# Optimization experiments

Hardware: AMD Instinct MI355X
Metric: run time of the kernel (lower is better)

Reference implementation:

```python
import jax, jax.numpy as jnp
import numpy as np

B, T, E, H = 64, 512, 256, 128


def setup_inputs() -> dict:
    key = jax.random.key(0)
    ks = jax.random.split(key, 7)
    s = 1.0 / np.sqrt(H)  # PyTorch LSTM default init range
    inputs = jax.random.normal(ks[0], (B, T, E), jnp.float32)
    labels = jax.random.randint(ks[1], (B, T), 0, H)
    W_ih = jax.random.uniform(ks[2], (4 * H, E), jnp.float32, -s, s)
    W_hh = jax.random.uniform(ks[3], (4 * H, H), jnp.float32, -s, s)
    b_ih = jax.random.uniform(ks[4], (4 * H,), jnp.float32, -s, s)
    b_hh = jax.random.uniform(ks[5], (4 * H,), jnp.float32, -s, s)
    transition = jax.random.uniform(ks[6], (H, H), jnp.float32)  # torch.rand
    return {"inputs": inputs, "labels": labels, "W_ih": W_ih, "W_hh": W_hh,
            "b_ih": b_ih, "b_hh": b_hh, "transition": transition}


def _lstm(x, W_ih, W_hh, b_ih, b_hh):
    # x: (T, B, E) -> hs: (T, B, H). PyTorch gate order: i, f, g, o.
    Bn = x.shape[1]
    Hn = W_hh.shape[1]

    def step(carry, xt):
        h, c = carry
        g = xt @ W_ih.T + b_ih + h @ W_hh.T + b_hh  # (B, 4H)
        i, f, gg, o = jnp.split(g, 4, axis=-1)
        c = jax.nn.sigmoid(f) * c + jax.nn.sigmoid(i) * jnp.tanh(gg)
        h = jax.nn.sigmoid(o) * jnp.tanh(c)
        return (h, c), h

    h0 = jnp.zeros((Bn, Hn), x.dtype)
    (_, _), hs = jax.lax.scan(step, (h0, h0), x)
    return hs


def reference(inputs, labels, W_ih, W_hh, b_ih, b_hh, transition):
    x = inputs.transpose(1, 0, 2)  # (T, B, E)
    trans = jax.nn.softmax(transition, axis=1)  # row-softmax transition
    hs = _lstm(x, W_ih, W_hh, b_ih, b_hh)  # (T, B, H)
    Hbth = jax.nn.softmax(hs, axis=2).transpose(1, 0, 2)  # (B, T, H)

    # gold-path score Pr: emissions at gold tags + transition scores
    emit = jnp.take_along_axis(Hbth, labels[:, :, None], axis=2)[..., 0].sum(axis=1)  # (B,)
    tr_score = trans[labels[:, :-1], labels[:, 1:]].sum(axis=1)  # (B,)
    Pr = emit + tr_score

    # CRF forward algorithm (partition score Ps) via scan over time
    pre0 = Hbth[:, 0, :] + trans[0]  # (B, H)

    def crf_step(pre, h_t):
        # Z[b, i, j] = pre[b, i] + trans[i, j] + h_t[b, j]
        Z = pre[:, :, None] + trans[None] + h_t[:, None, :]
        return jax.nn.logsumexp(Z, axis=1), None

    pre, _ = jax.lax.scan(crf_step, pre0, Hbth[:, 1:, :].transpose(1, 0, 2))
    Ps = jax.nn.logsumexp(pre + trans[-1][None, :], axis=1)  # (B,)

    return (Ps - Pr).sum()
```

## Files before the change

### kernel.cpp

```cpp
#include <hip/hip_runtime.h>
#include <hip/hip_bf16.h>
#include <cstdint>

#define BB 64
#define TT 512
#define EE 256
#define HH 128
#define G4 512

typedef _Float16 half2_t __attribute__((ext_vector_type(2)));
typedef _Float16 f16x4 __attribute__((ext_vector_type(4)));
typedef _Float16 f16x8 __attribute__((ext_vector_type(8)));
typedef float f32x4 __attribute__((ext_vector_type(4)));

#define BC(x) __builtin_bit_cast(half2_t, x)

#define BAR() asm volatile("s_waitcnt lgkmcnt(0)\n\ts_barrier" ::: "memory")

__device__ __forceinline__ float fdot2f(half2_t a, half2_t b, float c) {
#if defined(__has_builtin)
#if __has_builtin(__builtin_amdgcn_fdot2)
  return __builtin_amdgcn_fdot2(a, b, c, false);
#else
  return c + (float)a[0] * (float)b[0] + (float)a[1] * (float)b[1];
#endif
#else
  return c + (float)a[0] * (float)b[0] + (float)a[1] * (float)b[1];
#endif
}

__device__ __forceinline__ float rcp_(float x) { return __builtin_amdgcn_rcpf(x); }
__device__ __forceinline__ float sigmoid_(float x) { return rcp_(1.f + __expf(-x)); }
__device__ __forceinline__ float tanh_(float x) {
  float ax = fabsf(x);
  float e = __expf(-2.f * ax);
  float r = (1.f - e) * rcp_(1.f + e);
  return copysignf(r, x);
}

__device__ __forceinline__ float readlane_f(float x, int lane) {
#if defined(__has_builtin)
#if __has_builtin(__builtin_amdgcn_readlane)
  return __builtin_bit_cast(float, __builtin_amdgcn_readlane(__builtin_bit_cast(int, x), lane));
#else
  return __shfl(x, lane);
#endif
#else
  return __shfl(x, lane);
#endif
}

#if defined(__has_builtin)
#if __has_builtin(__builtin_amdgcn_update_dpp)
#define HAVE_DPP 1
#endif
#endif

__device__ __forceinline__ float wave_sum64_bcast(float x) {
#ifdef HAVE_DPP
#define DPP_ADD(ctrl)                                                          \
  {                                                                            \
    int _t = __builtin_amdgcn_update_dpp(0, __builtin_bit_cast(int, x), ctrl,  \
                                         0xf, 0xf, true);                      \
    x += __builtin_bit_cast(float, _t);                                        \
  }
  DPP_ADD(0x111)
  DPP_ADD(0x112)
  DPP_ADD(0x114)
  DPP_ADD(0x118)
  DPP_ADD(0x142)
  DPP_ADD(0x143)
#undef DPP_ADD
  return readlane_f(x, 63);
#else
#pragma unroll
  for (int s = 1; s <= 32; s <<= 1) x += __shfl_xor(x, s);
  return x;
#endif
}

__device__ __host__ __forceinline__ int permj(int j) {
  return ((j & 127) << 2) | (j >> 7);
}

__global__ __launch_bounds__(128) void prep_kernel(
    const float* __restrict__ transition, const float* __restrict__ W_ih,
    float* __restrict__ trans, _Float16* __restrict__ W16) {
  const int bid = blockIdx.x, t = threadIdx.x;
  if (bid < 128) {
    __shared__ float red[2];
    float v = transition[bid * HH + t];
    float m = v;
#pragma unroll
    for (int s = 32; s >= 1; s >>= 1) m = fmaxf(m, __shfl_xor(m, s));
    if ((t & 63) == 0) red[t >> 6] = m;
    __syncthreads();
    m = fmaxf(red[0], red[1]);
    float e = __expf(v - m);
    float s = e;
#pragma unroll
    for (int k = 32; k >= 1; k >>= 1) s += __shfl_xor(s, k);
    __syncthreads();
    if ((t & 63) == 0) red[t >> 6] = s;
    __syncthreads();
    trans[bid * HH + t] = e * rcp_(red[0] + red[1]);
  } else {
    const int base = (bid - 128) * 1024 + t * 8;
    const int row = base >> 8;
    const int col = base & 255;
    float4 v0 = *(const float4*)(W_ih + base);
    float4 v1 = *(const float4*)(W_ih + base + 4);
    f16x8 h;
    h[0] = (_Float16)v0.x; h[1] = (_Float16)v0.y;
    h[2] = (_Float16)v0.z; h[3] = (_Float16)v0.w;
    h[4] = (_Float16)v1.x; h[5] = (_Float16)v1.y;
    h[6] = (_Float16)v1.z; h[7] = (_Float16)v1.w;
    *(f16x8*)(W16 + (size_t)permj(row) * EE + col) = h;
  }
}

__global__ __launch_bounds__(256) void gemm_in(
    const float* __restrict__ A, const _Float16* __restrict__ W16,
    const float* __restrict__ b_ih, const float* __restrict__ b_hh,
    float* __restrict__ out) {
  __shared__ _Float16 As[64][264];
  const int t = threadIdx.x;
  const int m0 = blockIdx.x * 64;
  const int n0 = blockIdx.y * 256;
  {
    const int c4 = t & 63, r0 = t >> 6;
#pragma unroll
    for (int p = 0; p < 16; ++p) {
      const int row = r0 + 4 * p;
      float4 v = *(const float4*)(A + (size_t)(m0 + row) * EE + c4 * 4);
      f16x4 h;
      h[0] = (_Float16)v.x; h[1] = (_Float16)v.y;
      h[2] = (_Float16)v.z; h[3] = (_Float16)v.w;
      *(f16x4*)&As[row][c4 * 4] = h;
    }
  }
  __syncthreads();
  const int w = t >> 6, L = t & 63;
  const int lrow = L & 15, quad = L >> 4, lk = quad * 8;
  f32x4 acc[4][4] = {};
  const _Float16* Wbase = W16 + (size_t)(n0 + w * 64) * EE;
#pragma unroll
  for (int kc = 0; kc < 8; ++kc) {
    f16x8 a[4], bf[4];
#pragma unroll
    for (int mf = 0; mf < 4; ++mf)
      a[mf] = *(const f16x8*)&As[mf * 16 + lrow][kc * 32 + lk];
#pragma unroll
    for (int nf = 0; nf < 4; ++nf)
      bf[nf] = *(const f16x8*)(Wbase + (size_t)(nf * 16 + lrow) * EE + kc * 32 + lk);
#pragma unroll
    for (int mf = 0; mf < 4; ++mf)
#pragma unroll
      for (int nf = 0; nf < 4; ++nf)
        acc[mf][nf] = __builtin_amdgcn_mfma_f32_16x16x32_f16(a[mf], bf[nf], acc[mf][nf], 0, 0, 0);
  }
#pragma unroll
  for (int nf = 0; nf < 4; ++nf) {
    const int j = n0 + w * 64 + nf * 16 + lrow;
    const int jo = ((j & 3) << 7) | (j >> 2);
    const float bias = b_ih[jo] + b_hh[jo];
#pragma unroll
    for (int mf = 0; mf < 4; ++mf) {
#pragma unroll
      for (int r = 0; r < 4; ++r) {
        const int m = m0 + mf * 16 + quad * 4 + r;
        out[(size_t)m * G4 + j] = acc[mf][nf][r] + bias;
      }
    }
  }
}

__global__ __launch_bounds__(512, 1) void lstm_crf(
    const float* __restrict__ precomp, const float* __restrict__ Whh,
    const float* __restrict__ trans, const int* __restrict__ labels,
    float* __restrict__ out_b) {
  const int b = blockIdx.x, t = threadIdx.x;
  const int w = t >> 6, l = t & 63, q = l >> 4, l15 = l & 15;
  const int tf_a = l15 & 3;
  const int gg = l15 >> 2;
  const int ua = 16 * w + 4 * tf_a + q;
  const int g2 = t >> 7, jj = t & 127;

  __shared__ __align__(16) _Float16 h_lds[2][HH];
  __shared__ __align__(16) _Float16 E_lds[HH];
  __shared__ __align__(16) float act[G4];
  __shared__ __align__(16) float Spart[G4];
  __shared__ int lab[TT];

  f16x8 wfr[4][4];
#pragma unroll
  for (int tf = 0; tf < 4; ++tf) {
    const int rowp = 16 * (4 * w + tf) + l15;
    const int u = rowp >> 2, g = rowp & 3;
    const float* src = Whh + (size_t)(g * HH + u) * HH;
#pragma unroll
    for (int kt = 0; kt < 4; ++kt) {
      const float* s8 = src + kt * 32 + q * 8;
      float4 v0 = *(const float4*)s8;
      float4 v1 = *(const float4*)(s8 + 4);
      f16x8 h8;
      h8[0] = (_Float16)v0.x; h8[1] = (_Float16)v0.y;
      h8[2] = (_Float16)v0.z; h8[3] = (_Float16)v0.w;
      h8[4] = (_Float16)v1.x; h8[5] = (_Float16)v1.y;
      h8[6] = (_Float16)v1.z; h8[7] = (_Float16)v1.w;
      wfr[tf][kt] = h8;
    }
  }
  half2_t et[16];
#pragma unroll
  for (int a = 0; a < 16; ++a) {
    float e0 = __expf(trans[(g2 * 32 + 2 * a) * HH + jj]);
    float e1 = __expf(trans[(g2 * 32 + 2 * a + 1) * HH + jj]);
    half2_t h2; h2[0] = (_Float16)e0; h2[1] = (_Float16)e1;
    et[a] = h2;
  }
  lab[t] = labels[b * TT + t];
  if (t < HH) { h_lds[0][t] = (_Float16)0.f; E_lds[t] = (_Float16)0.f; }

  float tr0x = 0.f, tr0y = 0.f, tr127x = 0.f, tr127y = 0.f;
  if (t < 64) {
    float2 v0 = *(const float2*)(trans + 2 * t);
    float2 v1 = *(const float2*)(trans + 127 * HH + 2 * t);
    tr0x = v0.x; tr0y = v0.y; tr127x = v1.x; tr127y = v1.y;
  }
  float c0 = 0.f, c1 = 0.f, preA = 0.f, preB = 0.f, mused = 0.f, emit = 0.f;

  const float* pcb = precomp + (size_t)b * TT * G4 + 64 * w + 4 * q;
  f32x4 pc_cur[4], pc_nxt[4];
#pragma unroll
  for (int tf = 0; tf < 4; ++tf) pc_cur[tf] = *(const f32x4*)(pcb + 16 * tf);
  __syncthreads();

#pragma unroll 1
  for (int step = 0; step < TT; ++step) {
    const int pr = step & 1;
    const int sn = (step < TT - 1) ? step + 1 : step;
#pragma unroll
    for (int tf = 0; tf < 4; ++tf)
      pc_nxt[tf] = *(const f32x4*)(pcb + (size_t)sn * G4 + 16 * tf);
    const f16x8 hb0 = *(const f16x8*)&h_lds[pr][q * 8];
    const f16x8 hb1 = *(const f16x8*)&h_lds[pr][32 + q * 8];
    const f16x8 hb2 = *(const f16x8*)&h_lds[pr][64 + q * 8];
    const f16x8 hb3 = *(const f16x8*)&h_lds[pr][96 + q * 8];
    f32x4 a0 = pc_cur[0], a1 = pc_cur[1], a2 = pc_cur[2], a3 = pc_cur[3];
    a0 = __builtin_amdgcn_mfma_f32_16x16x32_f16(wfr[0][0], hb0, a0, 0, 0, 0);
    a1 = __builtin_amdgcn_mfma_f32_16x16x32_f16(wfr[1][0], hb0, a1, 0, 0, 0);
    a2 = __builtin_amdgcn_mfma_f32_16x16x32_f16(wfr[2][0], hb0, a2, 0, 0, 0);
    a3 = __builtin_amdgcn_mfma_f32_16x16x32_f16(wfr[3][0], hb0, a3, 0, 0, 0);
    a0 = __builtin_amdgcn_mfma_f32_16x16x32_f16(wfr[0][1], hb1, a0, 0, 0, 0);
    a1 = __builtin_amdgcn_mfma_f32_16x16x32_f16(wfr[1][1], hb1, a1, 0, 0, 0);
    a2 = __builtin_amdgcn_mfma_f32_16x16x32_f16(wfr[2][1], hb1, a2, 0, 0, 0);
    a3 = __builtin_amdgcn_mfma_f32_16x16x32_f16(wfr[3][1], hb1, a3, 0, 0, 0);
    a0 = __builtin_amdgcn_mfma_f32_16x16x32_f16(wfr[0][2], hb2, a0, 0, 0, 0);
    a1 = __builtin_amdgcn_mfma_f32_16x16x32_f16(wfr[1][2], hb2, a1, 0, 0, 0);
    a2 = __builtin_amdgcn_mfma_f32_16x16x32_f16(wfr[2][2], hb2, a2, 0, 0, 0);
    a3 = __builtin_amdgcn_mfma_f32_16x16x32_f16(wfr[3][2], hb2, a3, 0, 0, 0);
    a0 = __builtin_amdgcn_mfma_f32_16x16x32_f16(wfr[0][3], hb3, a0, 0, 0, 0);
    a1 = __builtin_amdgcn_mfma_f32_16x16x32_f16(wfr[1][3], hb3, a1, 0, 0, 0);
    a2 = __builtin_amdgcn_mfma_f32_16x16x32_f16(wfr[2][3], hb3, a2, 0, 0, 0);
    a3 = __builtin_amdgcn_mfma_f32_16x16x32_f16(wfr[3][3], hb3, a3, 0, 0, 0);
    float s0 = 0.f, s1 = 0.f;
    const float4* ev4 = (const float4*)E_lds + g2 * 4;
#pragma unroll
    for (int ec = 0; ec < 4; ++ec) {
      float4 eb = ev4[ec];
      s0 = fdot2f(et[4 * ec + 0], BC(eb.x), s0);
      s1 = fdot2f(et[4 * ec + 1], BC(eb.y), s1);
      s0 = fdot2f(et[4 * ec + 2], BC(eb.z), s0);
      s1 = fdot2f(et[4 * ec + 3], BC(eb.w), s1);
    }
    const f32x4 asel = (tf_a == 0) ? a0 : (tf_a == 1) ? a1 : (tf_a == 2) ? a2 : a3;
    const float gv = (gg == 0) ? asel[0] : (gg == 1) ? asel[1]
                   : (gg == 2) ? asel[2] : asel[3];
    const bool isg = (gg == 2);
    const float yy = isg ? (-2.f * fabsf(gv)) : (-gv);
    const float exv = __expf(yy);
    const float num = isg ? (1.f - exv) : 1.f;
    float av = num * rcp_(1.f + exv);
    av = isg ? copysignf(av, gv) : av;
    act[gg * HH + ua] = av;
    Spart[t] = s0 + s1;
    BAR();
    if (t < 64) {
      const float2* a2p = (const float2*)act;
      float2 I = a2p[t], F = a2p[64 + t], G = a2p[128 + t], O = a2p[192 + t];
      c0 = F.x * c0 + I.x * G.x;
      c1 = F.y * c1 + I.y * G.y;
      const float h0 = O.x * tanh_(c0), h1 = O.y * tanh_(c1);
      const float e0 = __expf(h0), e1 = __expf(h1);
      const float denom = wave_sum64_bcast(e0 + e1);
      const float rinv = rcp_(denom);
      const float p0 = e0 * rinv, p1 = e1 * rinv;
      const float2* s2p = (const float2*)Spart;
      float2 Sq0 = s2p[t], Sq1 = s2p[64 + t], Sq2 = s2p[128 + t], Sq3 = s2p[192 + t];
      const float Sa = (Sq0.x + Sq1.x) + (Sq2.x + Sq3.x);
      const float Sb = (Sq0.y + Sq1.y) + (Sq2.y + Sq3.y);
      const float lgSa = __logf(Sa), lgSb = __logf(Sb);
      const float lgS0 = readlane_f(lgSa, 0);
      const int lb = lab[step];
      const float Mnext = (step == 0) ? 0.f : (mused + lgS0);
      preA = p0 + ((step == 0) ? tr0x : (mused + lgSa));
      preB = p1 + ((step == 0) ? tr0y : (mused + lgSb));
      if (2 * t == lb) emit += p0;
      if (2 * t + 1 == lb) emit += p1;
      half2_t Eh;
      Eh[0] = (_Float16)__expf(preA - Mnext);
      Eh[1] = (_Float16)__expf(preB - Mnext);
      *(half2_t*)&E_lds[2 * t] = Eh;
      half2_t Hh;
      Hh[0] = (_Float16)h0; Hh[1] = (_Float16)h1;
      *(half2_t*)&h_lds[pr ^ 1][2 * t] = Hh;
      mused = Mnext;
    }
    BAR();
#pragma unroll
    for (int tf = 0; tf < 4; ++tf) pc_cur[tf] = pc_nxt[tf];
  }
  if (t < 64) {
    float v0 = preA + tr127x, v1 = preB + tr127y;
    float m = fmaxf(v0, v1);
#pragma unroll
    for (int s = 1; s <= 32; s <<= 1) m = fmaxf(m, __shfl_xor(m, s));
    float ex = __expf(v0 - m) + __expf(v1 - m);
    float em = emit;
#pragma unroll
    for (int s = 1; s <= 32; s <<= 1) {
      ex += __shfl_xor(ex, s);
      em += __shfl_xor(em, s);
    }
    if (t == 0) out_b[b] = m + __logf(ex) - em;
  }
}

__global__ __launch_bounds__(512) void finalize_kernel(
    const float* __restrict__ trans, const int* __restrict__ labels,
    const float* __restrict__ out_b, float* __restrict__ d_out) {
  const int t = threadIdx.x;
  float a = 0.f;
  if (t < TT - 1) {
    for (int b = 0; b < BB; ++b) {
      const int l0 = labels[b * TT + t];
      const int l1 = labels[b * TT + t + 1];
      a += trans[l0 * HH + l1];
    }
  }
  float x = ((t < BB) ? out_b[t] : 0.f) - a;
  __shared__ float red[8];
#pragma unroll
  for (int s = 32; s >= 1; s >>= 1) x += __shfl_xor(x, s);
  if ((t & 63) == 0) red[t >> 6] = x;
  __syncthreads();
  if (t == 0) {
    float s = 0.f;
#pragma unroll
    for (int i = 0; i < 8; ++i) s += red[i];
    d_out[0] = s;
  }
}

extern "C" void kernel_launch(void* const* d_in, const int* in_sizes, int n_in,
                              void* d_out, int out_size, void* d_ws, size_t ws_size,
                              hipStream_t stream) {
  const float* inputs = (const float*)d_in[0];
  const int* labels = (const int*)d_in[1];
  const float* W_ih = (const float*)d_in[2];
  const float* W_hh = (const float*)d_in[3];
  const float* b_ih = (const float*)d_in[4];
  const float* b_hh = (const float*)d_in[5];
  const float* transition = (const float*)d_in[6];

  char* ws = (char*)d_ws;
  float* precomp = (float*)ws;
  float* trans = (float*)(ws + 67108864);
  _Float16* W16 = (_Float16*)(ws + 67108864 + 65536);
  float* out_b = (float*)(ws + 67108864 + 65536 + 262144);

  prep_kernel<<<256, 128, 0, stream>>>(transition, W_ih, trans, W16);
  gemm_in<<<dim3(512, 2), 256, 0, stream>>>(inputs, W16, b_ih, b_hh, precomp);
  lstm_crf<<<64, 512, 0, stream>>>(precomp, W_hh, trans, labels, out_b);
  finalize_kernel<<<1, 512, 0, stream>>>(trans, labels, out_b, (float*)d_out);
}
```

Measured before the change: 563.1 us.

## Split LSTM and CRF into dedicated waves, pipelined with one barrier per step

The fused kernel gets two extra waves that run the CRF forward recursion one timestep behind the LSTM waves, so the two recurrences overlap. Each step now needs a single barrier instead of two. The LSTM cell update is done in-register with DPP lane shifts across the gate lanes, which removes the act/Spart LDS round trip and the single-wave serial cell update. The costs are 64 half2 transition registers per CRF lane, an extra pipeline step, and a 4-deep h ring buffer in both fp16 and fp32.

```diff
diff --git a/kernel.cpp b/kernel.cpp
--- a/kernel.cpp
+++ b/kernel.cpp
@@ -30,7 +30,6 @@
 }
 
 __device__ __forceinline__ float rcp_(float x) { return __builtin_amdgcn_rcpf(x); }
-__device__ __forceinline__ float sigmoid_(float x) { return rcp_(1.f + __expf(-x)); }
 __device__ __forceinline__ float tanh_(float x) {
   float ax = fabsf(x);
   float e = __expf(-2.f * ax);
@@ -54,6 +53,14 @@
 #if __has_builtin(__builtin_amdgcn_update_dpp)
 #define HAVE_DPP 1
 #endif
+#endif
+
+#ifdef HAVE_DPP
+#define DPP_SHL(dst, src, N)                                                   \
+  dst = __builtin_bit_cast(float, __builtin_amdgcn_update_dpp(                 \
+            0, __builtin_bit_cast(int, src), 0x100 | (N), 0xf, 0xf, true))
+#else
+#define DPP_SHL(dst, src, N) dst = __shfl((src), (threadIdx.x & 63) + (N))
 #endif
 
 __device__ __forceinline__ float wave_sum64_bcast(float x) {
@@ -175,7 +182,7 @@
   }
 }
 
-__global__ __launch_bounds__(512, 1) void lstm_crf(
+__global__ __launch_bounds__(640, 1) void lstm_crf(
     const float* __restrict__ precomp, const float* __restrict__ Whh,
     const float* __restrict__ trans, const int* __restrict__ labels,
     float* __restrict__ out_b) {
@@ -183,158 +190,175 @@
   const int w = t >> 6, l = t & 63, q = l >> 4, l15 = l & 15;
   const int tf_a = l15 & 3;
   const int gg = l15 >> 2;
-  const int ua = 16 * w + 4 * tf_a + q;
-  const int g2 = t >> 7, jj = t & 127;
-
-  __shared__ __align__(16) _Float16 h_lds[2][HH];
-  __shared__ __align__(16) _Float16 E_lds[HH];
-  __shared__ __align__(16) float act[G4];
-  __shared__ __align__(16) float Spart[G4];
+  const bool isL = (w < 8);
+  const int cw = w - 8;
+  const int j = cw * 64 + l;
+
+  __shared__ __align__(16) _Float16 h16[4][HH];
+  __shared__ __align__(16) float h32[4][HH];
+  __shared__ __align__(16) _Float16 E16[2][HH];
+  __shared__ float Mld[2][2];
+  __shared__ float fin[8];
   __shared__ int lab[TT];
 
   f16x8 wfr[4][4];
-#pragma unroll
-  for (int tf = 0; tf < 4; ++tf) {
-    const int rowp = 16 * (4 * w + tf) + l15;
-    const int u = rowp >> 2, g = rowp & 3;
-    const float* src = Whh + (size_t)(g * HH + u) * HH;
-#pragma unroll
-    for (int kt = 0; kt < 4; ++kt) {
-      const float* s8 = src + kt * 32 + q * 8;
-      float4 v0 = *(const float4*)s8;
-      float4 v1 = *(const float4*)(s8 + 4);
-      f16x8 h8;
-      h8[0] = (_Float16)v0.x; h8[1] = (_Float16)v0.y;
-      h8[2] = (_Float16)v0.z; h8[3] = (_Float16)v0.w;
-      h8[4] = (_Float16)v1.x; h8[5] = (_Float16)v1.y;
-      h8[6] = (_Float16)v1.z; h8[7] = (_Float16)v1.w;
-      wfr[tf][kt] = h8;
-    }
-  }
-  half2_t et[16];
-#pragma unroll
-  for (int a = 0; a < 16; ++a) {
-    float e0 = __expf(trans[(g2 * 32 + 2 * a) * HH + jj]);
-    float e1 = __expf(trans[(g2 * 32 + 2 * a + 1) * HH + jj]);
-    half2_t h2; h2[0] = (_Float16)e0; h2[1] = (_Float16)e1;
-    et[a] = h2;
-  }
-  lab[t] = labels[b * TT + t];
-  if (t < HH) { h_lds[0][t] = (_Float16)0.f; E_lds[t] = (_Float16)0.f; }
-
-  float tr0x = 0.f, tr0y = 0.f, tr127x = 0.f, tr127y = 0.f;
-  if (t < 64) {
-    float2 v0 = *(const float2*)(trans + 2 * t);
-    float2 v1 = *(const float2*)(trans + 127 * HH + 2 * t);
-    tr0x = v0.x; tr0y = v0.y; tr127x = v1.x; tr127y = v1.y;
-  }
-  float c0 = 0.f, c1 = 0.f, preA = 0.f, preB = 0.f, mused = 0.f, emit = 0.f;
-
-  const float* pcb = precomp + (size_t)b * TT * G4 + 64 * w + 4 * q;
   f32x4 pc_cur[4], pc_nxt[4];
-#pragma unroll
-  for (int tf = 0; tf < 4; ++tf) pc_cur[tf] = *(const f32x4*)(pcb + 16 * tf);
+  const float* pcb = nullptr;
+  float c = 0.f;
+  half2_t et[64];
+  float tr0 = 0.f, tr127 = 0.f, pre = 0.f, emit = 0.f;
+
+  if (isL) {
+#pragma unroll
+    for (int tf = 0; tf < 4; ++tf) {
+      const int rowp = 16 * (4 * w + tf) + l15;
+      const int u = rowp >> 2, g = rowp & 3;
+      const float* src = Whh + (size_t)(g * HH + u) * HH;
+#pragma unroll
+      for (int kt = 0; kt < 4; ++kt) {
+        const float* s8 = src + kt * 32 + q * 8;
+        float4 v0 = *(const float4*)s8;
+        float4 v1 = *(const float4*)(s8 + 4);
+        f16x8 h8;
+        h8[0] = (_Float16)v0.x; h8[1] = (_Float16)v0.y;
+        h8[2] = (_Float16)v0.z; h8[3] = (_Float16)v0.w;
+        h8[4] = (_Float16)v1.x; h8[5] = (_Float16)v1.y;
+        h8[6] = (_Float16)v1.z; h8[7] = (_Float16)v1.w;
+        wfr[tf][kt] = h8;
+      }
+    }
+    pcb = precomp + (size_t)b * TT * G4 + 64 * w + 4 * q;
+#pragma unroll
+    for (int tf = 0; tf < 4; ++tf) pc_cur[tf] = *(const f32x4*)(pcb + 16 * tf);
+  } else {
+#pragma unroll
+    for (int i = 0; i < 64; ++i) {
+      float e0 = __expf(trans[(2 * i) * HH + j]);
+      float e1 = __expf(trans[(2 * i + 1) * HH + j]);
+      half2_t h2; h2[0] = (_Float16)e0; h2[1] = (_Float16)e1;
+      et[i] = h2;
+    }
+    tr0 = trans[j];
+    tr127 = trans[127 * HH + j];
+  }
+  if (t < TT) lab[t] = labels[b * TT + t];
+  if (t < HH) { h16[0][t] = (_Float16)0.f; h32[0][t] = 0.f; }
   __syncthreads();
 
 #pragma unroll 1
-  for (int step = 0; step < TT; ++step) {
-    const int pr = step & 1;
-    const int sn = (step < TT - 1) ? step + 1 : step;
-#pragma unroll
-    for (int tf = 0; tf < 4; ++tf)
-      pc_nxt[tf] = *(const f32x4*)(pcb + (size_t)sn * G4 + 16 * tf);
-    const f16x8 hb0 = *(const f16x8*)&h_lds[pr][q * 8];
-    const f16x8 hb1 = *(const f16x8*)&h_lds[pr][32 + q * 8];
-    const f16x8 hb2 = *(const f16x8*)&h_lds[pr][64 + q * 8];
-    const f16x8 hb3 = *(const f16x8*)&h_lds[pr][96 + q * 8];
-    f32x4 a0 = pc_cur[0], a1 = pc_cur[1], a2 = pc_cur[2], a3 = pc_cur[3];
-    a0 = __builtin_amdgcn_mfma_f32_16x16x32_f16(wfr[0][0], hb0, a0, 0, 0, 0);
-    a1 = __builtin_amdgcn_mfma_f32_16x16x32_f16(wfr[1][0], hb0, a1, 0, 0, 0);
-    a2 = __builtin_amdgcn_mfma_f32_16x16x32_f16(wfr[2][0], hb0, a2, 0, 0, 0);
-    a3 = __builtin_amdgcn_mfma_f32_16x16x32_f16(wfr[3][0], hb0, a3, 0, 0, 0);
-    a0 = __builtin_amdgcn_mfma_f32_16x16x32_f16(wfr[0][1], hb1, a0, 0, 0, 0);
-    a1 = __builtin_amdgcn_mfma_f32_16x16x32_f16(wfr[1][1], hb1, a1, 0, 0, 0);
-    a2 = __builtin_amdgcn_mfma_f32_16x16x32_f16(wfr[2][1], hb1, a2, 0, 0, 0);
-    a3 = __builtin_amdgcn_mfma_f32_16x16x32_f16(wfr[3][1], hb1, a3, 0, 0, 0);
-    a0 = __builtin_amdgcn_mfma_f32_16x16x32_f16(wfr[0][2], hb2, a0, 0, 0, 0);
-    a1 = __builtin_amdgcn_mfma_f32_16x16x32_f16(wfr[1][2], hb2, a1, 0, 0, 0);
-    a2 = __builtin_amdgcn_mfma_f32_16x16x32_f16(wfr[2][2], hb2, a2, 0, 0, 0);
-    a3 = __builtin_amdgcn_mfma_f32_16x16x32_f16(wfr[3][2], hb2, a3, 0, 0, 0);
-    a0 = __builtin_amdgcn_mfma_f32_16x16x32_f16(wfr[0][3], hb3, a0, 0, 0, 0);
-    a1 = __builtin_amdgcn_mfma_f32_16x16x32_f16(wfr[1][3], hb3, a1, 0, 0, 0);
-    a2 = __builtin_amdgcn_mfma_f32_16x16x32_f16(wfr[2][3], hb3, a2, 0, 0, 0);
-    a3 = __builtin_amdgcn_mfma_f32_16x16x32_f16(wfr[3][3], hb3, a3, 0, 0, 0);
-    float s0 = 0.f, s1 = 0.f;
-    const float4* ev4 = (const float4*)E_lds + g2 * 4;
-#pragma unroll
-    for (int ec = 0; ec < 4; ++ec) {
-      float4 eb = ev4[ec];
-      s0 = fdot2f(et[4 * ec + 0], BC(eb.x), s0);
-      s1 = fdot2f(et[4 * ec + 1], BC(eb.y), s1);
-      s0 = fdot2f(et[4 * ec + 2], BC(eb.z), s0);
-      s1 = fdot2f(et[4 * ec + 3], BC(eb.w), s1);
-    }
-    const f32x4 asel = (tf_a == 0) ? a0 : (tf_a == 1) ? a1 : (tf_a == 2) ? a2 : a3;
-    const float gv = (gg == 0) ? asel[0] : (gg == 1) ? asel[1]
-                   : (gg == 2) ? asel[2] : asel[3];
-    const bool isg = (gg == 2);
-    const float yy = isg ? (-2.f * fabsf(gv)) : (-gv);
-    const float exv = __expf(yy);
-    const float num = isg ? (1.f - exv) : 1.f;
-    float av = num * rcp_(1.f + exv);
-    av = isg ? copysignf(av, gv) : av;
-    act[gg * HH + ua] = av;
-    Spart[t] = s0 + s1;
+  for (int s = 0; s <= TT; ++s) {
+    if (isL) {
+      if (s < TT) {
+        const int sn = (s < TT - 1) ? s + 1 : s;
+#pragma unroll
+        for (int tf = 0; tf < 4; ++tf)
+          pc_nxt[tf] = *(const f32x4*)(pcb + (size_t)sn * G4 + 16 * tf);
+        const int rs = s & 3;
+        const f16x8 hb0 = *(const f16x8*)&h16[rs][q * 8];
+        const f16x8 hb1 = *(const f16x8*)&h16[rs][32 + q * 8];
+        const f16x8 hb2 = *(const f16x8*)&h16[rs][64 + q * 8];
+        const f16x8 hb3 = *(const f16x8*)&h16[rs][96 + q * 8];
+        f32x4 a0 = pc_cur[0], a1 = pc_cur[1], a2 = pc_cur[2], a3 = pc_cur[3];
+        a0 = __builtin_amdgcn_mfma_f32_16x16x32_f16(wfr[0][0], hb0, a0, 0, 0, 0);
+        a1 = __builtin_amdgcn_mfma_f32_16x16x32_f16(wfr[1][0], hb0, a1, 0, 0, 0);
+        a2 = __builtin_amdgcn_mfma_f32_16x16x32_f16(wfr[2][0], hb0, a2, 0, 0, 0);
+        a3 = __builtin_amdgcn_mfma_f32_16x16x32_f16(wfr[3][0], hb0, a3, 0, 0, 0);
+        a0 = __builtin_amdgcn_mfma_f32_16x16x32_f16(wfr[0][1], hb1, a0, 0, 0, 0);
+        a1 = __builtin_amdgcn_mfma_f32_16x16x32_f16(wfr[1][1], hb1, a1, 0, 0, 0);
+        a2 = __builtin_amdgcn_mfma_f32_16x16x32_f16(wfr[2][1], hb1, a2, 0, 0, 0);
+        a3 = __builtin_amdgcn_mfma_f32_16x16x32_f16(wfr[3][1], hb1, a3, 0, 0, 0);
+        a0 = __builtin_amdgcn_mfma_f32_16x16x32_f16(wfr[0][2], hb2, a0, 0, 0, 0);
+        a1 = __builtin_amdgcn_mfma_f32_16x16x32_f16(wfr[1][2], hb2, a1, 0, 0, 0);
+        a2 = __builtin_amdgcn_mfma_f32_16x16x32_f16(wfr[2][2], hb2, a2, 0, 0, 0);
+        a3 = __builtin_amdgcn_mfma_f32_16x16x32_f16(wfr[3][2], hb2, a3, 0, 0, 0);
+        a0 = __builtin_amdgcn_mfma_f32_16x16x32_f16(wfr[0][3], hb3, a0, 0, 0, 0);
+        a1 = __builtin_amdgcn_mfma_f32_16x16x32_f16(wfr[1][3], hb3, a1, 0, 0, 0);
+        a2 = __builtin_amdgcn_mfma_f32_16x16x32_f16(wfr[2][3], hb3, a2, 0, 0, 0);
+        a3 = __builtin_amdgcn_mfma_f32_16x16x32_f16(wfr[3][3], hb3, a3, 0, 0, 0);
+        const f32x4 asel = (tf_a == 0) ? a0 : (tf_a == 1) ? a1 : (tf_a == 2) ? a2 : a3;
+        const float gv = (gg == 0) ? asel[0] : (gg == 1) ? asel[1]
+                       : (gg == 2) ? asel[2] : asel[3];
+        const bool isg = (gg == 2);
+        const float yy = isg ? (-2.f * fabsf(gv)) : (-gv);
+        const float exv = __expf(yy);
+        const float num = isg ? (1.f - exv) : 1.f;
+        float av = num * rcp_(1.f + exv);
+        av = isg ? copysignf(av, gv) : av;
+        float Fv, Gv, Ov;
+        DPP_SHL(Fv, av, 4);
+        DPP_SHL(Gv, av, 8);
+        DPP_SHL(Ov, av, 12);
+        c = Fv * c + av * Gv;
+        const float hv = Ov * tanh_(c);
+        if (gg == 0) {
+          const int ua = 16 * w + 4 * l15 + q;
+          h16[(s + 1) & 3][ua] = (_Float16)hv;
+          h32[(s + 1) & 3][ua] = hv;
+        }
+#pragma unroll
+        for (int tf = 0; tf < 4; ++tf) pc_cur[tf] = pc_nxt[tf];
+      }
+    } else if (s >= 1) {
+      const int rs = s & 3;
+      const float2 hp = *(const float2*)&h32[rs][2 * l];
+      const float denom = wave_sum64_bcast(__expf(hp.x) + __expf(hp.y));
+      const float hj = h32[rs][j];
+      const float p = __expf(hj) * rcp_(denom);
+      if (s == 1) {
+        pre = p + tr0;
+      } else {
+        const int rp = (s & 1) ^ 1;
+        float Slo = 0.f, Shi = 0.f;
+#pragma unroll
+        for (int ec = 0; ec < 8; ++ec) {
+          const float4 eb = *(const float4*)&E16[rp][ec * 8];
+          Slo = fdot2f(et[4 * ec + 0], BC(eb.x), Slo);
+          Slo = fdot2f(et[4 * ec + 1], BC(eb.y), Slo);
+          Slo = fdot2f(et[4 * ec + 2], BC(eb.z), Slo);
+          Slo = fdot2f(et[4 * ec + 3], BC(eb.w), Slo);
+        }
+#pragma unroll
+        for (int ec = 8; ec < 16; ++ec) {
+          const float4 eb = *(const float4*)&E16[rp][ec * 8];
+          Shi = fdot2f(et[4 * ec + 0], BC(eb.x), Shi);
+          Shi = fdot2f(et[4 * ec + 1], BC(eb.y), Shi);
+          Shi = fdot2f(et[4 * ec + 2], BC(eb.z), Shi);
+          Shi = fdot2f(et[4 * ec + 3], BC(eb.w), Shi);
+        }
+        const float Mlo = Mld[rp][0], Mhi = Mld[rp][1];
+        const float Cc = fmaxf(Mlo, Mhi);
+        const float lgS = Cc + __logf(__expf(Mlo - Cc) * Slo + __expf(Mhi - Cc) * Shi);
+        pre = p + lgS;
+      }
+      if (j == lab[s - 1]) emit += p;
+      const float Mw = readlane_f(pre, 0);
+      E16[s & 1][j] = (_Float16)__expf(pre - Mw);
+      if (l == 0) Mld[s & 1][cw] = Mw;
+    }
     BAR();
-    if (t < 64) {
-      const float2* a2p = (const float2*)act;
-      float2 I = a2p[t], F = a2p[64 + t], G = a2p[128 + t], O = a2p[192 + t];
-      c0 = F.x * c0 + I.x * G.x;
-      c1 = F.y * c1 + I.y * G.y;
-      const float h0 = O.x * tanh_(c0), h1 = O.y * tanh_(c1);
-      const float e0 = __expf(h0), e1 = __expf(h1);
-      const float denom = wave_sum64_bcast(e0 + e1);
-      const float rinv = rcp_(denom);
-      const float p0 = e0 * rinv, p1 = e1 * rinv;
-      const float2* s2p = (const float2*)Spart;
-      float2 Sq0 = s2p[t], Sq1 = s2p[64 + t], Sq2 = s2p[128 + t], Sq3 = s2p[192 + t];
-      const float Sa = (Sq0.x + Sq1.x) + (Sq2.x + Sq3.x);
-      const float Sb = (Sq0.y + Sq1.y) + (Sq2.y + Sq3.y);
-      const float lgSa = __logf(Sa), lgSb = __logf(Sb);
-      const float lgS0 = readlane_f(lgSa, 0);
-      const int lb = lab[step];
-      const float Mnext = (step == 0) ? 0.f : (mused + lgS0);
-      preA = p0 + ((step == 0) ? tr0x : (mused + lgSa));
-      preB = p1 + ((step == 0) ? tr0y : (mused + lgSb));
-      if (2 * t == lb) emit += p0;
-      if (2 * t + 1 == lb) emit += p1;
-      half2_t Eh;
-      Eh[0] = (_Float16)__expf(preA - Mnext);
-      Eh[1] = (_Float16)__expf(preB - Mnext);
-      *(half2_t*)&E_lds[2 * t] = Eh;
-      half2_t Hh;
-      Hh[0] = (_Float16)h0; Hh[1] = (_Float16)h1;
-      *(half2_t*)&h_lds[pr ^ 1][2 * t] = Hh;
-      mused = Mnext;
-    }
-    BAR();
-#pragma unroll
-    for (int tf = 0; tf < 4; ++tf) pc_cur[tf] = pc_nxt[tf];
-  }
-  if (t < 64) {
-    float v0 = preA + tr127x, v1 = preB + tr127y;
-    float m = fmaxf(v0, v1);
-#pragma unroll
-    for (int s = 1; s <= 32; s <<= 1) m = fmaxf(m, __shfl_xor(m, s));
-    float ex = __expf(v0 - m) + __expf(v1 - m);
+  }
+  if (!isL) {
+    float v = pre + tr127;
+    float m = v;
+#pragma unroll
+    for (int s2 = 1; s2 <= 32; s2 <<= 1) m = fmaxf(m, __shfl_xor(m, s2));
+    if (l == 0) fin[cw] = m;
+  }
+  __syncthreads();
+  if (!isL) {
+    const float M2 = fmaxf(fin[0], fin[1]);
+    float ex = __expf(pre + tr127 - M2);
     float em = emit;
 #pragma unroll
-    for (int s = 1; s <= 32; s <<= 1) {
-      ex += __shfl_xor(ex, s);
-      em += __shfl_xor(em, s);
-    }
-    if (t == 0) out_b[b] = m + __logf(ex) - em;
-  }
+    for (int s2 = 1; s2 <= 32; s2 <<= 1) {
+      ex += __shfl_xor(ex, s2);
+      em += __shfl_xor(em, s2);
+    }
+    if (l == 0) { fin[2 + cw] = ex; fin[4 + cw] = em; }
+  }
+  __syncthreads();
+  if (t == 0)
+    out_b[b] = fmaxf(fin[0], fin[1]) + __logf(fin[2] + fin[3]) - (fin[4] + fin[5]);
 }
 
 __global__ __launch_bounds__(512) void finalize_kernel(
@@ -382,6 +406,6 @@
 
   prep_kernel<<<256, 128, 0, stream>>>(transition, W_ih, trans, W16);
   gemm_in<<<dim3(512, 2), 256, 0, stream>>>(inputs, W16, b_ih, b_hh, precomp);
-  lstm_crf<<<64, 512, 0, stream>>>(precomp, W_hh, trans, labels, out_b);
+  lstm_crf<<<64, 640, 0, stream>>>(precomp, W_hh, trans, labels, out_b);
   finalize_kernel<<<1, 512, 0, stream>>>(trans, labels, out_b, (float*)d_out);
 }
```

Result: slower. 1.295 ms (+130.0%).

## Compute LSTM cell update in all waves via DPP lane shifts

Applied to the files above, without the earlier changes.

The LSTM cell-state update, tanh and exp of h now run distributed across all eight waves. Each wave pulls the forget, g and output gate values from neighbouring lanes with DPP row shifts, so the gate activations no longer round-trip through an LDS act array to a single wave. Each wave writes its h values and exp(h) to LDS and stores a per-wave partial softmax sum. Wave 0 then only adds the eight partials and finishes the CRF step, which shortens the serial section between barriers at the cost of extra LDS writes and a reduction in every wave.

```diff
diff --git a/kernel.cpp b/kernel.cpp
--- a/kernel.cpp
+++ b/kernel.cpp
@@ -30,7 +30,6 @@
 }
 
 __device__ __forceinline__ float rcp_(float x) { return __builtin_amdgcn_rcpf(x); }
-__device__ __forceinline__ float sigmoid_(float x) { return rcp_(1.f + __expf(-x)); }
 __device__ __forceinline__ float tanh_(float x) {
   float ax = fabsf(x);
   float e = __expf(-2.f * ax);
@@ -54,6 +53,14 @@
 #if __has_builtin(__builtin_amdgcn_update_dpp)
 #define HAVE_DPP 1
 #endif
+#endif
+
+#ifdef HAVE_DPP
+#define DPP_SHL(dst, src, N)                                                   \
+  dst = __builtin_bit_cast(float, __builtin_amdgcn_update_dpp(                 \
+            0, __builtin_bit_cast(int, src), 0x100 | (N), 0xf, 0xf, true))
+#else
+#define DPP_SHL(dst, src, N) dst = __shfl((src), (threadIdx.x & 63) + (N))
 #endif
 
 __device__ __forceinline__ float wave_sum64_bcast(float x) {
@@ -183,13 +190,13 @@
   const int w = t >> 6, l = t & 63, q = l >> 4, l15 = l & 15;
   const int tf_a = l15 & 3;
   const int gg = l15 >> 2;
-  const int ua = 16 * w + 4 * tf_a + q;
   const int g2 = t >> 7, jj = t & 127;
 
-  __shared__ __align__(16) _Float16 h_lds[2][HH];
+  __shared__ __align__(16) _Float16 h16[2][HH];
+  __shared__ __align__(16) float e32[2][HH];
   __shared__ __align__(16) _Float16 E_lds[HH];
-  __shared__ __align__(16) float act[G4];
   __shared__ __align__(16) float Spart[G4];
+  __shared__ __align__(16) float ws[8];
   __shared__ int lab[TT];
 
   f16x8 wfr[4][4];
@@ -220,7 +227,7 @@
     et[a] = h2;
   }
   lab[t] = labels[b * TT + t];
-  if (t < HH) { h_lds[0][t] = (_Float16)0.f; E_lds[t] = (_Float16)0.f; }
+  if (t < HH) { h16[0][t] = (_Float16)0.f; E_lds[t] = (_Float16)0.f; }
 
   float tr0x = 0.f, tr0y = 0.f, tr127x = 0.f, tr127y = 0.f;
   if (t < 64) {
@@ -228,7 +235,8 @@
     float2 v1 = *(const float2*)(trans + 127 * HH + 2 * t);
     tr0x = v0.x; tr0y = v0.y; tr127x = v1.x; tr127y = v1.y;
   }
-  float c0 = 0.f, c1 = 0.f, preA = 0.f, preB = 0.f, mused = 0.f, emit = 0.f;
+  float c = 0.f;
+  float preA = 0.f, preB = 0.f, mused = 0.f, emit = 0.f;
 
   const float* pcb = precomp + (size_t)b * TT * G4 + 64 * w + 4 * q;
   f32x4 pc_cur[4], pc_nxt[4];
@@ -243,10 +251,10 @@
 #pragma unroll
     for (int tf = 0; tf < 4; ++tf)
       pc_nxt[tf] = *(const f32x4*)(pcb + (size_t)sn * G4 + 16 * tf);
-    const f16x8 hb0 = *(const f16x8*)&h_lds[pr][q * 8];
-    const f16x8 hb1 = *(const f16x8*)&h_lds[pr][32 + q * 8];
-    const f16x8 hb2 = *(const f16x8*)&h_lds[pr][64 + q * 8];
-    const f16x8 hb3 = *(const f16x8*)&h_lds[pr][96 + q * 8];
+    const f16x8 hb0 = *(const f16x8*)&h16[pr][q * 8];
+    const f16x8 hb1 = *(const f16x8*)&h16[pr][32 + q * 8];
+    const f16x8 hb2 = *(const f16x8*)&h16[pr][64 + q * 8];
+    const f16x8 hb3 = *(const f16x8*)&h16[pr][96 + q * 8];
     f32x4 a0 = pc_cur[0], a1 = pc_cur[1], a2 = pc_cur[2], a3 = pc_cur[3];
     a0 = __builtin_amdgcn_mfma_f32_16x16x32_f16(wfr[0][0], hb0, a0, 0, 0, 0);
     a1 = __builtin_amdgcn_mfma_f32_16x16x32_f16(wfr[1][0], hb0, a1, 0, 0, 0);
@@ -283,19 +291,31 @@
     const float num = isg ? (1.f - exv) : 1.f;
     float av = num * rcp_(1.f + exv);
     av = isg ? copysignf(av, gv) : av;
-    act[gg * HH + ua] = av;
+    float Fv, Gv, Ov;
+    DPP_SHL(Fv, av, 4);
+    DPP_SHL(Gv, av, 8);
+    DPP_SHL(Ov, av, 12);
+    c = Fv * c + av * Gv;
+    const float hv = Ov * tanh_(c);
+    const float eh = __expf(hv);
+    if (gg == 0) {
+      const int ua = 16 * w + 4 * l15 + q;
+      h16[pr ^ 1][ua] = (_Float16)hv;
+      e32[pr ^ 1][ua] = eh;
+    }
+    float ehm = (gg == 0) ? eh : 0.f;
+    ehm = wave_sum64_bcast(ehm);
+    if (l == 0) ws[w] = ehm;
     Spart[t] = s0 + s1;
     BAR();
     if (t < 64) {
-      const float2* a2p = (const float2*)act;
-      float2 I = a2p[t], F = a2p[64 + t], G = a2p[128 + t], O = a2p[192 + t];
-      c0 = F.x * c0 + I.x * G.x;
-      c1 = F.y * c1 + I.y * G.y;
-      const float h0 = O.x * tanh_(c0), h1 = O.y * tanh_(c1);
-      const float e0 = __expf(h0), e1 = __expf(h1);
-      const float denom = wave_sum64_bcast(e0 + e1);
+      const float4 wsa = *(const float4*)ws;
+      const float4 wsb = *(const float4*)(ws + 4);
+      const float denom = ((wsa.x + wsa.y) + (wsa.z + wsa.w)) +
+                          ((wsb.x + wsb.y) + (wsb.z + wsb.w));
+      const float2 ep = *(const float2*)&e32[pr ^ 1][2 * t];
       const float rinv = rcp_(denom);
-      const float p0 = e0 * rinv, p1 = e1 * rinv;
+      const float p0 = ep.x * rinv, p1 = ep.y * rinv;
       const float2* s2p = (const float2*)Spart;
       float2 Sq0 = s2p[t], Sq1 = s2p[64 + t], Sq2 = s2p[128 + t], Sq3 = s2p[192 + t];
       const float Sa = (Sq0.x + Sq1.x) + (Sq2.x + Sq3.x);
@@ -312,9 +332,6 @@
       Eh[0] = (_Float16)__expf(preA - Mnext);
       Eh[1] = (_Float16)__expf(preB - Mnext);
       *(half2_t*)&E_lds[2 * t] = Eh;
-      half2_t Hh;
-      Hh[0] = (_Float16)h0; Hh[1] = (_Float16)h1;
-      *(half2_t*)&h_lds[pr ^ 1][2 * t] = Hh;
       mused = Mnext;
     }
     BAR();
```

After: 615.4 us. 1.09x slower.
